# Kernel optimization log

Measured on AMD Instinct MI355X. Metric: run time of the kernel, lower is better.

## Reference

```python
import jax, jax.numpy as jnp
import numpy as np

EMBED = 768
HIDDEN = 768
HEADS = 12
HEAD_DIM = HIDDEN // HEADS


def setup_inputs() -> dict:
    key = jax.random.key(0)
    ks = jax.random.split(key, 9)
    B, S = 16, 512
    lim = 1.0 / np.sqrt(EMBED)
    def lin(kw, kb):
        W = jax.random.uniform(kw, (EMBED, HIDDEN), jnp.float32, -lim, lim)
        b = jax.random.uniform(kb, (HIDDEN,), jnp.float32, -lim, lim)
        return W, b
    Wq, bq = lin(ks[0], ks[1])
    Wk, bk = lin(ks[2], ks[3])
    Wv, bv = lin(ks[4], ks[5])
    inp = jax.random.normal(ks[6], (B, S, EMBED), jnp.float32)
    mask = jax.random.randint(ks[7], (B, S), 0, 2).astype(jnp.float32)
    return {"input": inp, "input_mask": mask,
            "Wq": Wq, "bq": bq, "Wk": Wk, "bk": bk, "Wv": Wv, "bv": bv}


def reference(input, input_mask, Wq, bq, Wk, bk, Wv, bv):
    B, S, _ = input.shape
    # projections -> (B, H, S, D)
    def proj(W, b):
        x = jnp.einsum('bse,eh->bsh', input, W) + b
        return x.reshape(B, S, HEADS, HEAD_DIM).transpose(0, 2, 1, 3)
    Q = proj(Wq, bq)
    K = proj(Wk, bk)
    V = proj(Wv, bv)
    # scores (B, H, S, S), additive mask over keys
    scores = jnp.einsum('bhqd,bhkd->bhqk', Q, K) / jnp.sqrt(jnp.float32(HEAD_DIM))
    bias = (input_mask * -1e9)[:, None, None, :]  # (B,1,1,S) broadcast over heads & queries
    weight = jax.nn.softmax(scores + bias, axis=-1)
    out = jnp.einsum('bhqk,bhkd->bhqd', weight, V)
    return out.transpose(0, 2, 1, 3).reshape(B, S, HIDDEN)
```

## Files before the change

### kernel.cpp

```cpp
#include <hip/hip_runtime.h>
#include <cstdint>
#include <cstddef>

#define B_  16
#define S_  512
#define E_  768
#define NH_ 12
#define D_  64
#define M_  (B_*S_)

typedef unsigned short u16;
typedef __attribute__((ext_vector_type(4))) float f32x4;
typedef __attribute__((ext_vector_type(8))) short bf16x8;

#define LOG2E 1.4426950408889634f

__device__ __forceinline__ u16 f2bf(float f){
  union { float fv; uint32_t u; } v; v.fv = f;
  uint32_t u = v.u;
  uint32_t r = u + 0x7fffu + ((u >> 16) & 1u);
  return (u16)(r >> 16);
}

__device__ __forceinline__ void gload_lds16(const void* g, void* ldsbase){
  __builtin_amdgcn_global_load_lds(
      (const __attribute__((address_space(1))) unsigned int*)g,
      (__attribute__((address_space(3))) unsigned int*)ldsbase, 16, 0, 0);
}

__global__ __launch_bounds__(256) void cast_x_kernel(const float* __restrict__ x,
                                                     u16* __restrict__ xb, int n4){
  int i = blockIdx.x * 256 + threadIdx.x;
  if (i < n4){
    float4 v = reinterpret_cast<const float4*>(x)[i];
    ushort4 o;
    o.x = f2bf(v.x); o.y = f2bf(v.y); o.z = f2bf(v.z); o.w = f2bf(v.w);
    reinterpret_cast<ushort4*>(xb)[i] = o;
  }
}

__global__ __launch_bounds__(256) void transpose_w_kernel(const float* __restrict__ Wq,
                                                          const float* __restrict__ Wk,
                                                          const float* __restrict__ Wv,
                                                          u16* __restrict__ WtBase){
  __shared__ float t[32][33];
  const float* W = (blockIdx.z == 0) ? Wq : ((blockIdx.z == 1) ? Wk : Wv);
  u16* Wt = WtBase + (size_t)blockIdx.z * E_ * E_;
  int bx = blockIdx.x * 32, by = blockIdx.y * 32;
  int tx = threadIdx.x & 31, ty = threadIdx.x >> 5;
  #pragma unroll
  for (int i = 0; i < 32; i += 8)
    t[ty + i][tx] = W[(size_t)(by + ty + i) * E_ + bx + tx];
  __syncthreads();
  #pragma unroll
  for (int i = 0; i < 32; i += 8)
    Wt[(size_t)(bx + ty + i) * E_ + by + tx] = f2bf(t[tx][ty + i]);
}

__global__ __launch_bounds__(256) void qkv_gemm_kernel(
    const u16* __restrict__ Xb, const u16* __restrict__ WtBase,
    const float* __restrict__ bq, const float* __restrict__ bk, const float* __restrict__ bv,
    u16* __restrict__ Qb, u16* __restrict__ Kb, u16* __restrict__ VtB)
{
  __shared__ u16 lA[8 * 512];
  __shared__ u16 lB[8 * 512];
  const int z = blockIdx.z;
  const u16* Wt = WtBase + (size_t)z * E_ * E_;
  const float* bias = (z == 0) ? bq : ((z == 1) ? bk : bv);
  const int m0 = blockIdx.x * 128;
  const int n0 = blockIdx.y * 128;
  const int tid = threadIdx.x;
  const int lane = tid & 63;
  const int wave = tid >> 6;
  const int wm = wave & 1, wn = wave >> 1;
  const int ls = lane & 15;
  const int lk = lane >> 4;
  const int col0 = lane & 15, quad = lane >> 4;

  f32x4 acc[4][4];
  #pragma unroll
  for (int i = 0; i < 4; ++i)
    #pragma unroll
    for (int j = 0; j < 4; ++j)
      acc[i][j] = (f32x4){0.f, 0.f, 0.f, 0.f};

  #pragma unroll 1
  for (int k0 = 0; k0 < E_; k0 += 32){
    __syncthreads();
    #pragma unroll
    for (int cc = 0; cc < 2; ++cc){
      int c = wave * 2 + cc;
      gload_lds16(Xb + (size_t)(m0 + c*16 + ls) * E_ + k0 + lk*8, &lA[c*512]);
      gload_lds16(Wt + (size_t)(n0 + c*16 + ls) * E_ + k0 + lk*8, &lB[c*512]);
    }
    __syncthreads();
    bf16x8 af[4], bfr[4];
    #pragma unroll
    for (int mi = 0; mi < 4; ++mi)
      af[mi] = *reinterpret_cast<const bf16x8*>(&lA[(wm*4 + mi)*512 + lane*8]);
    #pragma unroll
    for (int ni = 0; ni < 4; ++ni)
      bfr[ni] = *reinterpret_cast<const bf16x8*>(&lB[(wn*4 + ni)*512 + lane*8]);
    #pragma unroll
    for (int mi = 0; mi < 4; ++mi)
      #pragma unroll
      for (int ni = 0; ni < 4; ++ni)
        acc[mi][ni] = __builtin_amdgcn_mfma_f32_16x16x32_bf16(af[mi], bfr[ni], acc[mi][ni], 0, 0, 0);
  }

  #pragma unroll
  for (int mi = 0; mi < 4; ++mi){
    #pragma unroll
    for (int ni = 0; ni < 4; ++ni){
      int n = n0 + wn*64 + ni*16 + col0;
      float bval = bias[n];
      int h = n >> 6, d = n & 63;
      #pragma unroll
      for (int r = 0; r < 4; ++r){
        int m = m0 + wm*64 + mi*16 + quad*4 + r;
        int b = m >> 9, s = m & 511;
        u16 obf = f2bf(acc[mi][ni][r] + bval);
        size_t bh = (size_t)b * NH_ + h;
        if (z == 0)      Qb[(bh * S_ + s) * D_ + d] = obf;
        else if (z == 1) Kb[(bh * S_ + s) * D_ + d] = obf;
        else             VtB[(bh * D_ + d) * S_ + s] = obf;
      }
    }
  }
}

__global__ __launch_bounds__(256) void attn_kernel(
    const u16* __restrict__ Qb, const u16* __restrict__ Kb, const u16* __restrict__ VtB,
    const float* __restrict__ mask, float* __restrict__ out)
{
  __shared__ u16 lK[8 * 512];
  __shared__ u16 lV[8 * 512];
  __shared__ u16 lP[4 * 1024];
  __shared__ float biasS[S_];
  const int qt = blockIdx.x;
  const int bh = blockIdx.y;
  const int b = bh / NH_, h = bh % NH_;
  const int tid = threadIdx.x, lane = tid & 63, wave = tid >> 6;
  const int col0 = lane & 15, quad = lane >> 4;
  const int ls = lane & 15, lk = lane >> 4;

  for (int i = tid; i < S_; i += 256)
    biasS[i] = mask[b * S_ + i] * -1e9f;

  const int qrow = qt*64 + wave*16 + col0;
  bf16x8 qf[2];
  #pragma unroll
  for (int ks = 0; ks < 2; ++ks)
    qf[ks] = *reinterpret_cast<const bf16x8*>(Qb + ((size_t)bh * S_ + qrow) * D_ + ks*32 + quad*8);

  f32x4 o[4];
  #pragma unroll
  for (int i = 0; i < 4; ++i) o[i] = (f32x4){0.f, 0.f, 0.f, 0.f};
  float mold = -3.0e38f;
  float lold = 0.f;

  #pragma unroll 1
  for (int st = 0; st < 8; ++st){
    __syncthreads();
    #pragma unroll
    for (int gg = 0; gg < 4; ++gg){
      int g = wave * 4 + gg;
      if (g < 8){
        int ks = g >> 2, nt = g & 3;
        gload_lds16(Kb + ((size_t)bh * S_ + st*64 + nt*16 + ls) * D_ + ks*32 + lk*8,
                    &lK[g*512]);
      } else {
        int g2 = g - 8;
        int ks2 = g2 >> 2, nd = g2 & 3;
        gload_lds16(VtB + ((size_t)bh * D_ + nd*16 + ls) * S_ + st*64 + ks2*32 + lk*8,
                    &lV[g2*512]);
      }
    }
    __syncthreads();

    f32x4 sc[4];
    #pragma unroll
    for (int nt = 0; nt < 4; ++nt) sc[nt] = (f32x4){0.f, 0.f, 0.f, 0.f};
    #pragma unroll
    for (int ks = 0; ks < 2; ++ks){
      #pragma unroll
      for (int nt = 0; nt < 4; ++nt){
        bf16x8 kf = *reinterpret_cast<const bf16x8*>(&lK[(ks*4 + nt)*512 + lane*8]);
        sc[nt] = __builtin_amdgcn_mfma_f32_16x16x32_bf16(kf, qf[ks], sc[nt], 0, 0, 0);
      }
    }
    float vv[4][4];
    #pragma unroll
    for (int nt = 0; nt < 4; ++nt){
      float4 bb = *reinterpret_cast<const float4*>(&biasS[st*64 + nt*16 + quad*4]);
      vv[nt][0] = sc[nt][0] * 0.125f + bb.x;
      vv[nt][1] = sc[nt][1] * 0.125f + bb.y;
      vv[nt][2] = sc[nt][2] * 0.125f + bb.z;
      vv[nt][3] = sc[nt][3] * 0.125f + bb.w;
    }
    float mrow = vv[0][0];
    #pragma unroll
    for (int nt = 0; nt < 4; ++nt)
      #pragma unroll
      for (int r = 0; r < 4; ++r)
        mrow = fmaxf(mrow, vv[nt][r]);
    mrow = fmaxf(mrow, __shfl_xor(mrow, 16, 64));
    mrow = fmaxf(mrow, __shfl_xor(mrow, 32, 64));
    float mnew = fmaxf(mold, mrow);
    float alpha = exp2f((mold - mnew) * LOG2E);
    float rsum = 0.f;
    #pragma unroll
    for (int nt = 0; nt < 4; ++nt){
      ushort4 pw;
      float p0 = exp2f((vv[nt][0] - mnew) * LOG2E);
      float p1 = exp2f((vv[nt][1] - mnew) * LOG2E);
      float p2 = exp2f((vv[nt][2] - mnew) * LOG2E);
      float p3 = exp2f((vv[nt][3] - mnew) * LOG2E);
      rsum += (p0 + p1) + (p2 + p3);
      pw.x = f2bf(p0); pw.y = f2bf(p1); pw.z = f2bf(p2); pw.w = f2bf(p3);
      int addr = wave*1024 + (nt >> 1)*512
               + (((nt & 1)*2 + (quad >> 1))*16 + col0)*8 + (quad & 1)*4;
      *reinterpret_cast<ushort4*>(&lP[addr]) = pw;
    }
    rsum += __shfl_xor(rsum, 16, 64);
    rsum += __shfl_xor(rsum, 32, 64);
    lold = alpha * lold + rsum;
    mold = mnew;
    #pragma unroll
    for (int r = 0; r < 4; ++r){
      float ar = __shfl(alpha, (lane & 48) | (quad*4 + r), 64);
      #pragma unroll
      for (int nd = 0; nd < 4; ++nd)
        o[nd][r] *= ar;
    }
    bf16x8 pf[2];
    #pragma unroll
    for (int ks2 = 0; ks2 < 2; ++ks2)
      pf[ks2] = *reinterpret_cast<const bf16x8*>(&lP[wave*1024 + ks2*512 + lane*8]);
    #pragma unroll
    for (int ks2 = 0; ks2 < 2; ++ks2){
      #pragma unroll
      for (int nd = 0; nd < 4; ++nd){
        bf16x8 vf = *reinterpret_cast<const bf16x8*>(&lV[(ks2*4 + nd)*512 + lane*8]);
        o[nd] = __builtin_amdgcn_mfma_f32_16x16x32_bf16(pf[ks2], vf, o[nd], 0, 0, 0);
      }
    }
  }

  #pragma unroll
  for (int r = 0; r < 4; ++r){
    int s = qt*64 + wave*16 + quad*4 + r;
    float lr = __shfl(lold, (lane & 48) | (quad*4 + r), 64);
    float inv = 1.0f / lr;
    #pragma unroll
    for (int nd = 0; nd < 4; ++nd){
      int d = nd*16 + col0;
      out[((size_t)b * S_ + s) * E_ + h*D_ + d] = o[nd][r] * inv;
    }
  }
}

extern "C" void kernel_launch(void* const* d_in, const int* in_sizes, int n_in,
                              void* d_out, int out_size, void* d_ws, size_t ws_size,
                              hipStream_t stream){
  const float* X    = (const float*)d_in[0];
  const float* mask = (const float*)d_in[1];
  const float* Wq   = (const float*)d_in[2];
  const float* bq   = (const float*)d_in[3];
  const float* Wk   = (const float*)d_in[4];
  const float* bk   = (const float*)d_in[5];
  const float* Wv   = (const float*)d_in[6];
  const float* bv   = (const float*)d_in[7];
  float* out = (float*)d_out;

  u16* Xb = (u16*)d_ws;
  u16* Wt = Xb + (size_t)M_ * E_;
  u16* Qb = Wt + (size_t)3 * E_ * E_;
  u16* Kb = Qb + (size_t)M_ * E_;
  u16* Vt = Kb + (size_t)M_ * E_;

  cast_x_kernel<<<(M_ * E_ / 4 + 255) / 256, 256, 0, stream>>>(X, Xb, M_ * E_ / 4);
  transpose_w_kernel<<<dim3(24, 24, 3), 256, 0, stream>>>(Wq, Wk, Wv, Wt);
  qkv_gemm_kernel<<<dim3(64, 6, 3), 256, 0, stream>>>(Xb, Wt, bq, bk, bv, Qb, Kb, Vt);
  attn_kernel<<<dim3(8, 192), 256, 0, stream>>>(Qb, Kb, Vt, mask, out);
}
```

Baseline: 214.4 us.

## Register-prefetch double-buffered tiles in QKV GEMM and attention, vectorize epilogue stores

Replaces direct global-to-LDS loads with register prefetch: the next k-tile (GEMM) or key/value block (attention) is loaded into registers while the current LDS tile is consumed, then written to LDS. The GEMM also double-buffers LDS, which removes one barrier per iteration. The GEMM swaps MFMA operand order so each lane holds four consecutive output columns, allowing float4 bias loads and packed ushort4 stores for Q/K. This raises register pressure and LDS use, which could lower occupancy.

```diff
diff --git a/kernel.cpp b/kernel.cpp
--- a/kernel.cpp
+++ b/kernel.cpp
@@ -20,12 +20,6 @@
   uint32_t u = v.u;
   uint32_t r = u + 0x7fffu + ((u >> 16) & 1u);
   return (u16)(r >> 16);
-}
-
-__device__ __forceinline__ void gload_lds16(const void* g, void* ldsbase){
-  __builtin_amdgcn_global_load_lds(
-      (const __attribute__((address_space(1))) unsigned int*)g,
-      (__attribute__((address_space(3))) unsigned int*)ldsbase, 16, 0, 0);
 }
 
 __global__ __launch_bounds__(256) void cast_x_kernel(const float* __restrict__ x,
@@ -62,8 +56,8 @@
     const float* __restrict__ bq, const float* __restrict__ bk, const float* __restrict__ bv,
     u16* __restrict__ Qb, u16* __restrict__ Kb, u16* __restrict__ VtB)
 {
-  __shared__ u16 lA[8 * 512];
-  __shared__ u16 lB[8 * 512];
+  __shared__ u16 lA[2][8 * 512];
+  __shared__ u16 lB[2][8 * 512];
   const int z = blockIdx.z;
   const u16* Wt = WtBase + (size_t)z * E_ * E_;
   const float* bias = (z == 0) ? bq : ((z == 1) ? bk : bv);
@@ -84,46 +78,66 @@
     for (int j = 0; j < 4; ++j)
       acc[i][j] = (f32x4){0.f, 0.f, 0.f, 0.f};
 
-  #pragma unroll 1
-  for (int k0 = 0; k0 < E_; k0 += 32){
-    __syncthreads();
+  uint4 rA[2], rB[2];
+  auto issue = [&](int k0){
     #pragma unroll
     for (int cc = 0; cc < 2; ++cc){
       int c = wave * 2 + cc;
-      gload_lds16(Xb + (size_t)(m0 + c*16 + ls) * E_ + k0 + lk*8, &lA[c*512]);
-      gload_lds16(Wt + (size_t)(n0 + c*16 + ls) * E_ + k0 + lk*8, &lB[c*512]);
+      rA[cc] = *reinterpret_cast<const uint4*>(Xb + (size_t)(m0 + c*16 + ls) * E_ + k0 + lk*8);
+      rB[cc] = *reinterpret_cast<const uint4*>(Wt + (size_t)(n0 + c*16 + ls) * E_ + k0 + lk*8);
+    }
+  };
+  issue(0);
+
+  #pragma unroll 2
+  for (int it = 0; it < 24; ++it){
+    const int cur = it & 1;
+    #pragma unroll
+    for (int cc = 0; cc < 2; ++cc){
+      int c = wave * 2 + cc;
+      *reinterpret_cast<uint4*>(&lA[cur][c*512 + lane*8]) = rA[cc];
+      *reinterpret_cast<uint4*>(&lB[cur][c*512 + lane*8]) = rB[cc];
     }
     __syncthreads();
-    bf16x8 af[4], bfr[4];
+    if (it + 1 < 24) issue((it + 1) * 32);
+    bf16x8 xf[4], wf[4];
     #pragma unroll
     for (int mi = 0; mi < 4; ++mi)
-      af[mi] = *reinterpret_cast<const bf16x8*>(&lA[(wm*4 + mi)*512 + lane*8]);
+      xf[mi] = *reinterpret_cast<const bf16x8*>(&lA[cur][(wm*4 + mi)*512 + lane*8]);
     #pragma unroll
     for (int ni = 0; ni < 4; ++ni)
-      bfr[ni] = *reinterpret_cast<const bf16x8*>(&lB[(wn*4 + ni)*512 + lane*8]);
+      wf[ni] = *reinterpret_cast<const bf16x8*>(&lB[cur][(wn*4 + ni)*512 + lane*8]);
     #pragma unroll
     for (int mi = 0; mi < 4; ++mi)
       #pragma unroll
       for (int ni = 0; ni < 4; ++ni)
-        acc[mi][ni] = __builtin_amdgcn_mfma_f32_16x16x32_bf16(af[mi], bfr[ni], acc[mi][ni], 0, 0, 0);
+        acc[mi][ni] = __builtin_amdgcn_mfma_f32_16x16x32_bf16(wf[ni], xf[mi], acc[mi][ni], 0, 0, 0);
   }
 
   #pragma unroll
   for (int mi = 0; mi < 4; ++mi){
+    int m = m0 + wm*64 + mi*16 + col0;
+    int b = m >> 9, s = m & 511;
     #pragma unroll
     for (int ni = 0; ni < 4; ++ni){
-      int n = n0 + wn*64 + ni*16 + col0;
-      float bval = bias[n];
-      int h = n >> 6, d = n & 63;
-      #pragma unroll
-      for (int r = 0; r < 4; ++r){
-        int m = m0 + wm*64 + mi*16 + quad*4 + r;
-        int b = m >> 9, s = m & 511;
-        u16 obf = f2bf(acc[mi][ni][r] + bval);
-        size_t bh = (size_t)b * NH_ + h;
-        if (z == 0)      Qb[(bh * S_ + s) * D_ + d] = obf;
-        else if (z == 1) Kb[(bh * S_ + s) * D_ + d] = obf;
-        else             VtB[(bh * D_ + d) * S_ + s] = obf;
+      int nbase = n0 + wn*64 + ni*16 + quad*4;
+      float4 bb = *reinterpret_cast<const float4*>(&bias[nbase]);
+      int h = nbase >> 6, d0 = nbase & 63;
+      size_t bh = (size_t)b * NH_ + h;
+      float v0 = acc[mi][ni][0] + bb.x;
+      float v1 = acc[mi][ni][1] + bb.y;
+      float v2 = acc[mi][ni][2] + bb.z;
+      float v3 = acc[mi][ni][3] + bb.w;
+      if (z < 2){
+        ushort4 pw;
+        pw.x = f2bf(v0); pw.y = f2bf(v1); pw.z = f2bf(v2); pw.w = f2bf(v3);
+        u16* dst = (z == 0) ? Qb : Kb;
+        *reinterpret_cast<ushort4*>(&dst[(bh * S_ + s) * D_ + d0]) = pw;
+      } else {
+        VtB[(bh * D_ + d0 + 0) * S_ + s] = f2bf(v0);
+        VtB[(bh * D_ + d0 + 1) * S_ + s] = f2bf(v1);
+        VtB[(bh * D_ + d0 + 2) * S_ + s] = f2bf(v2);
+        VtB[(bh * D_ + d0 + 3) * S_ + s] = f2bf(v3);
       }
     }
   }
@@ -153,6 +167,28 @@
   for (int ks = 0; ks < 2; ++ks)
     qf[ks] = *reinterpret_cast<const bf16x8*>(Qb + ((size_t)bh * S_ + qrow) * D_ + ks*32 + quad*8);
 
+  uint4 rg[4];
+  auto issue = [&](int st){
+    if (wave < 2){
+      #pragma unroll
+      for (int gg = 0; gg < 4; ++gg){
+        int g = wave*4 + gg;
+        int ks = g >> 2, nt = g & 3;
+        rg[gg] = *reinterpret_cast<const uint4*>(
+            Kb + ((size_t)bh * S_ + st*64 + nt*16 + ls) * D_ + ks*32 + lk*8);
+      }
+    } else {
+      #pragma unroll
+      for (int gg = 0; gg < 4; ++gg){
+        int g2 = (wave - 2)*4 + gg;
+        int ks2 = g2 >> 2, nd = g2 & 3;
+        rg[gg] = *reinterpret_cast<const uint4*>(
+            VtB + ((size_t)bh * D_ + nd*16 + ls) * S_ + st*64 + ks2*32 + lk*8);
+      }
+    }
+  };
+  issue(0);
+
   f32x4 o[4];
   #pragma unroll
   for (int i = 0; i < 4; ++i) o[i] = (f32x4){0.f, 0.f, 0.f, 0.f};
@@ -162,21 +198,17 @@
   #pragma unroll 1
   for (int st = 0; st < 8; ++st){
     __syncthreads();
-    #pragma unroll
-    for (int gg = 0; gg < 4; ++gg){
-      int g = wave * 4 + gg;
-      if (g < 8){
-        int ks = g >> 2, nt = g & 3;
-        gload_lds16(Kb + ((size_t)bh * S_ + st*64 + nt*16 + ls) * D_ + ks*32 + lk*8,
-                    &lK[g*512]);
-      } else {
-        int g2 = g - 8;
-        int ks2 = g2 >> 2, nd = g2 & 3;
-        gload_lds16(VtB + ((size_t)bh * D_ + nd*16 + ls) * S_ + st*64 + ks2*32 + lk*8,
-                    &lV[g2*512]);
-      }
+    if (wave < 2){
+      #pragma unroll
+      for (int gg = 0; gg < 4; ++gg)
+        *reinterpret_cast<uint4*>(&lK[(wave*4 + gg)*512 + lane*8]) = rg[gg];
+    } else {
+      #pragma unroll
+      for (int gg = 0; gg < 4; ++gg)
+        *reinterpret_cast<uint4*>(&lV[((wave - 2)*4 + gg)*512 + lane*8]) = rg[gg];
     }
     __syncthreads();
+    if (st < 7) issue(st + 1);
 
     f32x4 sc[4];
     #pragma unroll
```

After: 322.4 us. +50.4%, slower.

## Replace global_load_lds with register loads in GEMM and direct global K/V reads in attention

Applied to the files above, without the earlier changes.

The projection GEMM now stages tiles through registers and then writes them to LDS, instead of using the direct global-to-LDS load intrinsic. The attention kernel drops its K/V shared-memory staging and both per-tile barriers, and each wave loads its K and V fragments straight from global memory into registers. This removes the synchronisation and the LDS round-trip, but every wave in a block now fetches the same K/V tiles separately. That relies on L1/L2 caching to absorb the duplicated traffic, and the fragment arrays add register pressure.

```diff
diff --git a/kernel.cpp b/kernel.cpp
--- a/kernel.cpp
+++ b/kernel.cpp
@@ -20,12 +20,6 @@
   uint32_t u = v.u;
   uint32_t r = u + 0x7fffu + ((u >> 16) & 1u);
   return (u16)(r >> 16);
-}
-
-__device__ __forceinline__ void gload_lds16(const void* g, void* ldsbase){
-  __builtin_amdgcn_global_load_lds(
-      (const __attribute__((address_space(1))) unsigned int*)g,
-      (__attribute__((address_space(3))) unsigned int*)ldsbase, 16, 0, 0);
 }
 
 __global__ __launch_bounds__(256) void cast_x_kernel(const float* __restrict__ x,
@@ -87,11 +81,18 @@
   #pragma unroll 1
   for (int k0 = 0; k0 < E_; k0 += 32){
     __syncthreads();
+    uint4 va[2], vb[2];
     #pragma unroll
     for (int cc = 0; cc < 2; ++cc){
       int c = wave * 2 + cc;
-      gload_lds16(Xb + (size_t)(m0 + c*16 + ls) * E_ + k0 + lk*8, &lA[c*512]);
-      gload_lds16(Wt + (size_t)(n0 + c*16 + ls) * E_ + k0 + lk*8, &lB[c*512]);
+      va[cc] = *reinterpret_cast<const uint4*>(Xb + (size_t)(m0 + c*16 + ls) * E_ + k0 + lk*8);
+      vb[cc] = *reinterpret_cast<const uint4*>(Wt + (size_t)(n0 + c*16 + ls) * E_ + k0 + lk*8);
+    }
+    #pragma unroll
+    for (int cc = 0; cc < 2; ++cc){
+      int c = wave * 2 + cc;
+      *reinterpret_cast<uint4*>(&lA[c*512 + lane*8]) = va[cc];
+      *reinterpret_cast<uint4*>(&lB[c*512 + lane*8]) = vb[cc];
     }
     __syncthreads();
     bf16x8 af[4], bfr[4];
@@ -133,8 +134,6 @@
     const u16* __restrict__ Qb, const u16* __restrict__ Kb, const u16* __restrict__ VtB,
     const float* __restrict__ mask, float* __restrict__ out)
 {
-  __shared__ u16 lK[8 * 512];
-  __shared__ u16 lV[8 * 512];
   __shared__ u16 lP[4 * 1024];
   __shared__ float biasS[S_];
   const int qt = blockIdx.x;
@@ -142,10 +141,14 @@
   const int b = bh / NH_, h = bh % NH_;
   const int tid = threadIdx.x, lane = tid & 63, wave = tid >> 6;
   const int col0 = lane & 15, quad = lane >> 4;
-  const int ls = lane & 15, lk = lane >> 4;
+  const int ls = lane & 15;
 
   for (int i = tid; i < S_; i += 256)
     biasS[i] = mask[b * S_ + i] * -1e9f;
+  __syncthreads();
+
+  const u16* Kbh = Kb  + (size_t)bh * S_ * D_;
+  const u16* Vbh = VtB + (size_t)bh * D_ * S_;
 
   const int qrow = qt*64 + wave*16 + col0;
   bf16x8 qf[2];
@@ -161,34 +164,30 @@
 
   #pragma unroll 1
   for (int st = 0; st < 8; ++st){
-    __syncthreads();
-    #pragma unroll
-    for (int gg = 0; gg < 4; ++gg){
-      int g = wave * 4 + gg;
-      if (g < 8){
-        int ks = g >> 2, nt = g & 3;
-        gload_lds16(Kb + ((size_t)bh * S_ + st*64 + nt*16 + ls) * D_ + ks*32 + lk*8,
-                    &lK[g*512]);
-      } else {
-        int g2 = g - 8;
-        int ks2 = g2 >> 2, nd = g2 & 3;
-        gload_lds16(VtB + ((size_t)bh * D_ + nd*16 + ls) * S_ + st*64 + ks2*32 + lk*8,
-                    &lV[g2*512]);
-      }
-    }
-    __syncthreads();
+    bf16x8 kf[2][4];
+    #pragma unroll
+    for (int ks = 0; ks < 2; ++ks)
+      #pragma unroll
+      for (int nt = 0; nt < 4; ++nt)
+        kf[ks][nt] = *reinterpret_cast<const bf16x8*>(
+            Kbh + (size_t)(st*64 + nt*16 + ls) * D_ + ks*32 + quad*8);
+    bf16x8 vf[2][4];
+    #pragma unroll
+    for (int ks2 = 0; ks2 < 2; ++ks2)
+      #pragma unroll
+      for (int nd = 0; nd < 4; ++nd)
+        vf[ks2][nd] = *reinterpret_cast<const bf16x8*>(
+            Vbh + (size_t)(nd*16 + ls) * S_ + st*64 + ks2*32 + quad*8);
 
     f32x4 sc[4];
     #pragma unroll
     for (int nt = 0; nt < 4; ++nt) sc[nt] = (f32x4){0.f, 0.f, 0.f, 0.f};
     #pragma unroll
-    for (int ks = 0; ks < 2; ++ks){
-      #pragma unroll
-      for (int nt = 0; nt < 4; ++nt){
-        bf16x8 kf = *reinterpret_cast<const bf16x8*>(&lK[(ks*4 + nt)*512 + lane*8]);
-        sc[nt] = __builtin_amdgcn_mfma_f32_16x16x32_bf16(kf, qf[ks], sc[nt], 0, 0, 0);
-      }
-    }
+    for (int ks = 0; ks < 2; ++ks)
+      #pragma unroll
+      for (int nt = 0; nt < 4; ++nt)
+        sc[nt] = __builtin_amdgcn_mfma_f32_16x16x32_bf16(kf[ks][nt], qf[ks], sc[nt], 0, 0, 0);
+
     float vv[4][4];
     #pragma unroll
     for (int nt = 0; nt < 4; ++nt){
@@ -238,13 +237,10 @@
     for (int ks2 = 0; ks2 < 2; ++ks2)
       pf[ks2] = *reinterpret_cast<const bf16x8*>(&lP[wave*1024 + ks2*512 + lane*8]);
     #pragma unroll
-    for (int ks2 = 0; ks2 < 2; ++ks2){
-      #pragma unroll
-      for (int nd = 0; nd < 4; ++nd){
-        bf16x8 vf = *reinterpret_cast<const bf16x8*>(&lV[(ks2*4 + nd)*512 + lane*8]);
-        o[nd] = __builtin_amdgcn_mfma_f32_16x16x32_bf16(pf[ks2], vf, o[nd], 0, 0, 0);
-      }
-    }
+    for (int ks2 = 0; ks2 < 2; ++ks2)
+      #pragma unroll
+      for (int nd = 0; nd < 4; ++nd)
+        o[nd] = __builtin_amdgcn_mfma_f32_16x16x32_bf16(pf[ks2], vf[ks2][nd], o[nd], 0, 0, 0);
   }
 
   #pragma unroll
```

Result: slower. 280.5 us (+30.8%).
